# Optimization experiments

Hardware: AMD Instinct MI355X
Metric: run time of the kernel (lower is better)

## Reference

```python
import jax, jax.numpy as jnp
import numpy as np

# Module hyperparameters (n_heads must be 1 for the torch module's views to be consistent)
N_HEADS = 1
INPUT_DIM = 512
EMBED_DIM = 512
KEY_DIM = 512   # defaults: val_dim = embed_dim // n_heads, key_dim = val_dim
VAL_DIM = 512
INTERNAL = 80   # internal_node_holder
LEAF = 50       # leaf_node_holder
NEXT = 1        # next_holder
G = INTERNAL + LEAF + NEXT  # graph_size = 131
B = 512


def _uniform_init(k, shape):
    s = 1.0 / np.sqrt(shape[-1])
    return jax.random.uniform(k, shape, jnp.float32, -s, s)


def setup_inputs() -> dict:
    key = jax.random.key(0)
    ks = jax.random.split(key, 8)
    q = jax.random.normal(ks[0], (B * G, INPUT_DIM), jnp.float32)
    h = jax.random.normal(ks[1], (B, G, INPUT_DIM), jnp.float32)
    mask = jax.random.randint(ks[2], (B, G), 0, 2, jnp.int32)  # >0 means masked
    Wq = _uniform_init(ks[3], (KEY_DIM, INPUT_DIM))
    Wk = _uniform_init(ks[4], (KEY_DIM, INPUT_DIM))
    Wv = _uniform_init(ks[5], (VAL_DIM, INPUT_DIM))
    Wo = _uniform_init(ks[6], (EMBED_DIM, KEY_DIM))
    bo = _uniform_init(ks[7], (EMBED_DIM,))
    return {"q": q, "mask": mask, "graph_size": G, "evaluate": 0, "h": h,
            "Wq": Wq, "Wk": Wk, "Wv": Wv, "Wo": Wo, "bo": bo}


def reference(q, mask, graph_size, evaluate, h, Wq, Wk, Wv, Wo, bo):
    Gs = graph_size
    Bs = q.shape[0] // Gs
    norm = 1.0 / np.sqrt(KEY_DIM)

    # Projections (Linear, no bias). With n_heads=1 the (n_heads,B,N,-1) view is just (B,N,d).
    Q = (q @ Wq.T).reshape(Bs, Gs, KEY_DIM)                        # (B, G, dk)
    hflat = h.reshape(-1, INPUT_DIM)
    K = (hflat @ Wk.T).reshape(Bs, Gs, KEY_DIM)                    # (B, G, dk)
    V = (hflat @ Wv.T).reshape(Bs, Gs, VAL_DIM)                    # (B, G, dv)

    compatibility = norm * jnp.einsum('bqd,bkd->bqk', Q, K)       # (B, G, G)

    # mask (B,G) -> broadcast to (B,G,G); force the leaf-node block True
    idx = jnp.arange(Gs)
    mid = (idx >= INTERNAL) & (idx < Gs - NEXT)                    # leaf-node slots
    full_mask = (mask > 0)[:, None, :] | (mid[:, None] & mid[None, :])[None, :, :]

    fill = -jnp.inf if evaluate else -30.0
    compatibility = jnp.where(full_mask, fill, compatibility)
    attn = jax.nn.softmax(compatibility, axis=-1)
    attn = jnp.where(full_mask, 0.0, attn)                         # attnc zero-mask

    heads = jnp.einsum('bqk,bkd->bqd', attn, V)                    # (B, G, dv)
    out = heads.reshape(Bs * Gs, N_HEADS * VAL_DIM) @ Wo.T + bo    # (B*G, embed_dim)
    return out
```

## Files before the change

### kernel.cpp

```cpp
#include <hip/hip_runtime.h>
#include <hip/hip_bf16.h>

typedef short s16x8 __attribute__((ext_vector_type(8)));
typedef short s16x4 __attribute__((ext_vector_type(4)));
typedef float f32x4 __attribute__((ext_vector_type(4)));
typedef unsigned short u16;

#define MROWS 67072
#define GSZ   131
#define VT_KSTRIDE 160
#define VT_BATCH   (512 * VT_KSTRIDE)

__device__ inline u16 f2bf(float f) {
    return (u16)((__float_as_uint(f) + 0x8000u) >> 16);
}
__device__ inline unsigned pack2(float a, float b) {
    unsigned ua = __float_as_uint(a) + 0x8000u;
    unsigned ub = __float_as_uint(b) + 0x8000u;
    return (ua >> 16) | (ub & 0xFFFF0000u);
}
__device__ inline f32x4 mfma16(s16x8 a, s16x8 b, f32x4 c) {
    return __builtin_amdgcn_mfma_f32_16x16x32_bf16(a, b, c, 0, 0, 0);
}
typedef const __attribute__((address_space(1))) unsigned gas_u32;
typedef __attribute__((address_space(3))) unsigned las_u32;
__device__ inline void async16(const void* g, void* l) {
    __builtin_amdgcn_global_load_lds((gas_u32*)g, (las_u32*)l, 16, 0, 0);
}

__global__ __launch_bounds__(256)
void cvt_kernel(const float* __restrict__ src, u16* __restrict__ dst, int n8) {
    int i = blockIdx.x * 256 + threadIdx.x;
    if (i >= n8) return;
    const float4* s4 = (const float4*)src;
    float4 a = s4[2 * (size_t)i], b = s4[2 * (size_t)i + 1];
    union { s16x8 v; unsigned u[4]; } o;
    o.u[0] = pack2(a.x, a.y); o.u[1] = pack2(a.z, a.w);
    o.u[2] = pack2(b.x, b.y); o.u[3] = pack2(b.z, b.w);
    *(s16x8*)(dst + 8 * (size_t)i) = o.v;
}

template<int MODE>
__global__ __launch_bounds__(256, 2)
void gemm_bt(const u16* __restrict__ A, const u16* __restrict__ Bw,
             void* __restrict__ Outp, const float* __restrict__ bias)
{
    extern __shared__ __align__(16) char smem[];
    u16* smA = (u16*)smem;
    u16* smB = (u16*)(smem + 8192);
    u16* smC = (u16*)smem;

    const int tid  = threadIdx.x;
    const int lane = tid & 63;
    const int w    = tid >> 6;
    const int wm   = w >> 1, wn = w & 1;

    const int id    = (int)(blockIdx.x & 7) * 262 + (int)(blockIdx.x >> 3);
    const int mbase = (id >> 2) * 128;
    const int nbase = (id & 3) * 128;

    const int srow = w * 32 + (lane >> 2);
    const int scg  = (lane & 3) ^ (srow & 3);
    const u16* agp = A  + (size_t)(mbase + srow) * 512 + scg * 8;
    const u16* bgp = Bw + (size_t)(nbase + srow) * 512 + scg * 8;
    u16* al = smA + w * 1024;
    u16* bl = smB + w * 1024;

    f32x4 acc[4][4];
#pragma unroll
    for (int i = 0; i < 4; ++i)
#pragma unroll
        for (int j = 0; j < 4; ++j) acc[i][j] = (f32x4){0.f, 0.f, 0.f, 0.f};

    const int lr = lane & 15;
    const int co = ((lane >> 4) ^ (lr & 3)) * 8;

    for (int kk = 0; kk < 16; ++kk) {
        const int k0 = kk * 32;
        async16(agp + k0,            al);
        async16(agp + k0 + 16 * 512, al + 512);
        async16(bgp + k0,            bl);
        async16(bgp + k0 + 16 * 512, bl + 512);
        __syncthreads();

        s16x8 afr[4], bfr[4];
#pragma unroll
        for (int mi = 0; mi < 4; ++mi)
            afr[mi] = *(const s16x8*)&smA[(wm * 64 + mi * 16 + lr) * 32 + co];
#pragma unroll
        for (int ni = 0; ni < 4; ++ni)
            bfr[ni] = *(const s16x8*)&smB[(wn * 64 + ni * 16 + lr) * 32 + co];
#pragma unroll
        for (int mi = 0; mi < 4; ++mi)
#pragma unroll
            for (int ni = 0; ni < 4; ++ni)
                acc[mi][ni] = mfma16(afr[mi], bfr[ni], acc[mi][ni]);
        __syncthreads();
    }

    if constexpr (MODE == 2) {
        float bv[4];
#pragma unroll
        for (int ni = 0; ni < 4; ++ni) bv[ni] = bias[nbase + wn * 64 + ni * 16 + lr];
        float* outp = (float*)Outp;
#pragma unroll
        for (int mi = 0; mi < 4; ++mi)
#pragma unroll
            for (int ni = 0; ni < 4; ++ni) {
                int row0 = wm * 64 + mi * 16 + (lane >> 4) * 4;
                int col  = nbase + wn * 64 + ni * 16 + lr;
#pragma unroll
                for (int r = 0; r < 4; ++r)
                    outp[(size_t)(mbase + row0 + r) * 512 + col] = acc[mi][ni][r] + bv[ni];
            }
    } else if constexpr (MODE == 0) {
#pragma unroll
        for (int mi = 0; mi < 4; ++mi)
#pragma unroll
            for (int ni = 0; ni < 4; ++ni) {
                int row0 = wm * 64 + mi * 16 + (lane >> 4) * 4;
                int col  = wn * 64 + ni * 16 + lr;
#pragma unroll
                for (int r = 0; r < 4; ++r)
                    smC[(row0 + r) * 136 + col] = f2bf(acc[mi][ni][r]);
            }
        __syncthreads();
        u16* outp = (u16*)Outp;
        int rr = tid >> 1, cs = (tid & 1) * 64;
#pragma unroll
        for (int j = 0; j < 8; ++j) {
            s16x8 v = *(const s16x8*)&smC[rr * 136 + cs + j * 8];
            *(s16x8*)(outp + (size_t)(mbase + rr) * 512 + nbase + cs + j * 8) = v;
        }
    } else {
#pragma unroll
        for (int mi = 0; mi < 4; ++mi)
#pragma unroll
            for (int ni = 0; ni < 4; ++ni) {
                int nl = wn * 64 + ni * 16 + lr;
                int m0 = wm * 64 + mi * 16 + (lane >> 4) * 4;
                s16x4 pk;
#pragma unroll
                for (int r = 0; r < 4; ++r) pk[r] = (short)f2bf(acc[mi][ni][r]);
                *(s16x4*)&smC[nl * 136 + m0] = pk;
            }
        __syncthreads();
        u16* outp = (u16*)Outp;
        for (int i = 0; i < 32; ++i) {
            int n = w * 32 + i;
            int d = nbase + n;
#pragma unroll
            for (int hh = 0; hh < 2; ++hh) {
                int ml = hh * 64 + lane;
                unsigned mg = (unsigned)(mbase + ml);
                unsigned bb = mg / 131u;
                unsigned k2 = mg - bb * 131u;
                outp[(size_t)bb * VT_BATCH + (size_t)d * VT_KSTRIDE + k2] = smC[n * 136 + ml];
            }
        }
    }
}

__global__ __launch_bounds__(256, 4)
void attn_kernel(u16* __restrict__ QHb, const u16* __restrict__ Kb,
                 const u16* __restrict__ Vtb, const int* __restrict__ mask,
                 const int* __restrict__ evp)
{
    __shared__ __align__(16) u16 Qs[32 * 520];
    float* Ss = (float*)Qs;
    u16*   Ps = Qs + 9472;

    const int tid  = threadIdx.x;
    const int lane = tid & 63;
    const int w    = tid >> 6;
    const int id   = (int)(blockIdx.x & 7) * 320 + (int)(blockIdx.x >> 3);
    const int b    = id / 5;
    const int qt   = id - b * 5;
    const int q0   = qt * 32;
    const size_t rowbase = (size_t)b * GSZ;

    {
        int r = tid >> 3, cs = (tid & 7) * 64;
        int q = q0 + r;
        if (q < GSZ) {
            const u16* src = QHb + (rowbase + q) * 512 + cs;
#pragma unroll
            for (int j = 0; j < 8; ++j)
                *(s16x8*)&Qs[r * 520 + cs + j * 8] = *(const s16x8*)(src + j * 8);
        } else {
            s16x8 z = (s16x8){0,0,0,0,0,0,0,0};
#pragma unroll
            for (int j = 0; j < 8; ++j) *(s16x8*)&Qs[r * 520 + cs + j * 8] = z;
        }
    }
    __syncthreads();

    const int lr = lane & 15;
    const int lk = (lane >> 4) * 8;
    const float norm = 0.044194173824159216f;

    f32x4 sacc[3][2];
#pragma unroll
    for (int t = 0; t < 3; ++t) {
        sacc[t][0] = (f32x4){0.f,0.f,0.f,0.f};
        sacc[t][1] = (f32x4){0.f,0.f,0.f,0.f};
    }
#pragma unroll
    for (int t = 0; t < 3; ++t) {
        const int nt = w + 4 * t;
        if (nt < 9) {
            const u16* kbase = Kb + (rowbase + nt * 16 + lr) * 512 + lk;
#pragma unroll
            for (int ks = 0; ks < 16; ++ks) {
                s16x8 bfr = *(const s16x8*)(kbase + ks * 32);
                s16x8 a0  = *(const s16x8*)&Qs[(lr) * 520 + ks * 32 + lk];
                s16x8 a1  = *(const s16x8*)&Qs[(16 + lr) * 520 + ks * 32 + lk];
                sacc[t][0] = mfma16(a0, bfr, sacc[t][0]);
                sacc[t][1] = mfma16(a1, bfr, sacc[t][1]);
            }
        }
    }
    __syncthreads();

#pragma unroll
    for (int t = 0; t < 3; ++t) {
        const int nt = w + 4 * t;
        if (nt < 9) {
            int col = nt * 16 + lr;
            int rb  = (lane >> 4) * 4;
#pragma unroll
            for (int r = 0; r < 4; ++r) {
                Ss[(rb + r) * 148 + col]      = sacc[t][0][r] * norm;
                Ss[(16 + rb + r) * 148 + col] = sacc[t][1][r] * norm;
            }
        }
    }
    __syncthreads();

    {
        int r = tid >> 3, sub = tid & 7;
        int q = q0 + r;
        bool midq = (q >= 80) && (q < 130);
        int ev = *evp;
        float fill = ev ? -__builtin_inff() : -30.0f;
        float sv[17];
        float mx = -__builtin_inff();
#pragma unroll
        for (int j = 0; j < 17; ++j) {
            int k = sub + 8 * j;
            float s = -__builtin_inff();
            if (k < GSZ) {
                bool mk = (mask[b * GSZ + k] > 0) || (midq && (k >= 80) && (k < 130));
                s = mk ? fill : Ss[r * 148 + k];
            }
            sv[j] = s;
            mx = fmaxf(mx, s);
        }
#pragma unroll
        for (int off = 1; off < 8; off <<= 1) mx = fmaxf(mx, __shfl_xor(mx, off, 64));
        float sum = 0.f;
#pragma unroll
        for (int j = 0; j < 17; ++j) {
            int k = sub + 8 * j;
            if (k < GSZ) sum += __expf(sv[j] - mx);
        }
#pragma unroll
        for (int off = 1; off < 8; off <<= 1) sum += __shfl_xor(sum, off, 64);
        float inv = 1.0f / sum;
#pragma unroll
        for (int j = 0; j < 17; ++j) {
            int k = sub + 8 * j;
            if (k < GSZ) {
                bool mk = (mask[b * GSZ + k] > 0) || (midq && (k >= 80) && (k < 130));
                float p = mk ? 0.0f : __expf(sv[j] - mx) * inv;
                Ps[r * 168 + k] = f2bf(p);
            }
        }
        for (int k = GSZ + sub; k < 160; k += 8) Ps[r * 168 + k] = 0;
    }
    __syncthreads();

    f32x4 hacc[2][8];
#pragma unroll
    for (int mi = 0; mi < 2; ++mi)
#pragma unroll
        for (int ni = 0; ni < 8; ++ni) hacc[mi][ni] = (f32x4){0.f,0.f,0.f,0.f};
    const u16* vtbase = Vtb + (size_t)b * VT_BATCH + (size_t)(w * 128 + lr) * VT_KSTRIDE + lk;
#pragma unroll
    for (int kc = 0; kc < 5; ++kc) {
        s16x8 a0 = *(const s16x8*)&Ps[(lr) * 168 + kc * 32 + lk];
        s16x8 a1 = *(const s16x8*)&Ps[(16 + lr) * 168 + kc * 32 + lk];
#pragma unroll
        for (int ni = 0; ni < 8; ++ni) {
            s16x8 bfr = *(const s16x8*)(vtbase + (size_t)ni * 16 * VT_KSTRIDE + kc * 32);
            hacc[0][ni] = mfma16(a0, bfr, hacc[0][ni]);
            hacc[1][ni] = mfma16(a1, bfr, hacc[1][ni]);
        }
    }
    __syncthreads();

#pragma unroll
    for (int mi = 0; mi < 2; ++mi)
#pragma unroll
        for (int ni = 0; ni < 8; ++ni) {
            int row0 = mi * 16 + (lane >> 4) * 4;
            int col  = w * 128 + ni * 16 + lr;
#pragma unroll
            for (int r = 0; r < 4; ++r)
                Qs[(row0 + r) * 520 + col] = f2bf(hacc[mi][ni][r]);
        }
    __syncthreads();
    {
        int r = tid >> 3, cs = (tid & 7) * 64;
        int q = q0 + r;
        if (q < GSZ) {
            u16* dst = QHb + (rowbase + q) * 512 + cs;
#pragma unroll
            for (int j = 0; j < 8; ++j)
                *(s16x8*)(dst + j * 8) = *(const s16x8*)&Qs[r * 520 + cs + j * 8];
        }
    }
}

extern "C" void kernel_launch(void* const* d_in, const int* in_sizes, int n_in,
                              void* d_out, int out_size, void* d_ws, size_t ws_size,
                              hipStream_t stream) {
    const float* q    = (const float*)d_in[0];
    const int*   mask = (const int*)d_in[1];
    const int*   evp  = (const int*)d_in[3];
    const float* h    = (const float*)d_in[4];
    const float* Wq   = (const float*)d_in[5];
    const float* Wk   = (const float*)d_in[6];
    const float* Wv   = (const float*)d_in[7];
    const float* Wo   = (const float*)d_in[8];
    const float* bo   = (const float*)d_in[9];
    float* out = (float*)d_out;

    u16* Cbuf = (u16*)d_ws;
    u16* Kbuf = Cbuf + (size_t)MROWS * 512;
    u16* Qbuf = Kbuf + (size_t)MROWS * 512;
    u16* wWq  = Qbuf + (size_t)MROWS * 512;
    u16* wWk  = wWq + 512 * 512;
    u16* wWv  = wWk + 512 * 512;
    u16* wWo  = wWv + 512 * 512;
    u16* Vtb  = (u16*)d_out;

    const int n8_big = MROWS * 512 / 8;
    const int n8_w   = 512 * 512 / 8;
    dim3 bb(256);
    dim3 gcvt((n8_big + 255) / 256), gcw((n8_w + 255) / 256);
    dim3 gg(2096);
    const size_t lds_big = 34816, lds_min = 16384;

    cvt_kernel<<<gcw, bb, 0, stream>>>(Wq, wWq, n8_w);
    cvt_kernel<<<gcw, bb, 0, stream>>>(Wk, wWk, n8_w);
    cvt_kernel<<<gcw, bb, 0, stream>>>(Wv, wWv, n8_w);
    cvt_kernel<<<gcw, bb, 0, stream>>>(Wo, wWo, n8_w);

    cvt_kernel<<<gcvt, bb, 0, stream>>>(h, Cbuf, n8_big);
    gemm_bt<0><<<gg, bb, lds_big, stream>>>(Cbuf, wWk, (void*)Kbuf, nullptr);
    gemm_bt<1><<<gg, bb, lds_big, stream>>>(Cbuf, wWv, (void*)Vtb, nullptr);

    cvt_kernel<<<gcvt, bb, 0, stream>>>(q, Cbuf, n8_big);
    gemm_bt<0><<<gg, bb, lds_big, stream>>>(Cbuf, wWq, (void*)Qbuf, nullptr);

    attn_kernel<<<dim3(2560), bb, 0, stream>>>(Qbuf, Kbuf, Vtb, mask, evp);

    gemm_bt<2><<<gg, bb, lds_min, stream>>>(Qbuf, wWo, (void*)out, bo);
}
```

Baseline: 739.9 us.

## Prefetch K/V fragments and mask into registers in attention kernel

Loads the mask values into registers at kernel start, batches the K-fragment global loads eight at a time ahead of their MFMAs, and issues the first V-fragment loads before the softmax phase. The V loop is double-buffered so the next chunk is loaded while the current one is multiplied. Launch bounds drop from 4 to 3 blocks per SIMD to leave room for the extra registers, which may reduce occupancy.

```diff
diff --git a/kernel.cpp b/kernel.cpp
--- a/kernel.cpp
+++ b/kernel.cpp
@@ -161,7 +161,7 @@
     }
 }
 
-__global__ __launch_bounds__(256, 4)
+__global__ __launch_bounds__(256, 3)
 void attn_kernel(u16* __restrict__ QHb, const u16* __restrict__ Kb,
                  const u16* __restrict__ Vtb, const int* __restrict__ mask,
                  const int* __restrict__ evp)
@@ -179,18 +179,29 @@
     const int q0   = qt * 32;
     const size_t rowbase = (size_t)b * GSZ;
 
+    const int r8  = tid >> 3;
+    const int sub = tid & 7;
+
+    int ev = *evp;
+    int mkpre[17];
+#pragma unroll
+    for (int j = 0; j < 17; ++j) {
+        int k = sub + 8 * j;
+        mkpre[j] = (k < GSZ) ? mask[b * GSZ + k] : 1;
+    }
+
     {
-        int r = tid >> 3, cs = (tid & 7) * 64;
-        int q = q0 + r;
+        int cs = (tid & 7) * 64;
+        int q = q0 + r8;
         if (q < GSZ) {
             const u16* src = QHb + (rowbase + q) * 512 + cs;
 #pragma unroll
             for (int j = 0; j < 8; ++j)
-                *(s16x8*)&Qs[r * 520 + cs + j * 8] = *(const s16x8*)(src + j * 8);
+                *(s16x8*)&Qs[r8 * 520 + cs + j * 8] = *(const s16x8*)(src + j * 8);
         } else {
             s16x8 z = (s16x8){0,0,0,0,0,0,0,0};
 #pragma unroll
-            for (int j = 0; j < 8; ++j) *(s16x8*)&Qs[r * 520 + cs + j * 8] = z;
+            for (int j = 0; j < 8; ++j) *(s16x8*)&Qs[r8 * 520 + cs + j * 8] = z;
         }
     }
     __syncthreads();
@@ -198,6 +209,7 @@
     const int lr = lane & 15;
     const int lk = (lane >> 4) * 8;
     const float norm = 0.044194173824159216f;
+    const u16* vtbase = Vtb + (size_t)b * VT_BATCH + (size_t)(w * 128 + lr) * VT_KSTRIDE + lk;
 
     f32x4 sacc[3][2];
 #pragma unroll
@@ -211,15 +223,28 @@
         if (nt < 9) {
             const u16* kbase = Kb + (rowbase + nt * 16 + lr) * 512 + lk;
 #pragma unroll
-            for (int ks = 0; ks < 16; ++ks) {
-                s16x8 bfr = *(const s16x8*)(kbase + ks * 32);
-                s16x8 a0  = *(const s16x8*)&Qs[(lr) * 520 + ks * 32 + lk];
-                s16x8 a1  = *(const s16x8*)&Qs[(16 + lr) * 520 + ks * 32 + lk];
-                sacc[t][0] = mfma16(a0, bfr, sacc[t][0]);
-                sacc[t][1] = mfma16(a1, bfr, sacc[t][1]);
-            }
-        }
-    }
+            for (int h = 0; h < 2; ++h) {
+                s16x8 kf[8];
+#pragma unroll
+                for (int j = 0; j < 8; ++j)
+                    kf[j] = *(const s16x8*)(kbase + (h * 8 + j) * 32);
+#pragma unroll
+                for (int j = 0; j < 8; ++j) {
+                    const int ks = h * 8 + j;
+                    s16x8 a0 = *(const s16x8*)&Qs[(lr) * 520 + ks * 32 + lk];
+                    s16x8 a1 = *(const s16x8*)&Qs[(16 + lr) * 520 + ks * 32 + lk];
+                    sacc[t][0] = mfma16(a0, kf[j], sacc[t][0]);
+                    sacc[t][1] = mfma16(a1, kf[j], sacc[t][1]);
+                }
+            }
+        }
+    }
+
+    s16x8 vf[8];
+#pragma unroll
+    for (int j = 0; j < 8; ++j)
+        vf[j] = *(const s16x8*)(vtbase + (size_t)j * 16 * VT_KSTRIDE);
+
     __syncthreads();
 
 #pragma unroll
@@ -238,10 +263,8 @@
     __syncthreads();
 
     {
-        int r = tid >> 3, sub = tid & 7;
-        int q = q0 + r;
+        int q = q0 + r8;
         bool midq = (q >= 80) && (q < 130);
-        int ev = *evp;
         float fill = ev ? -__builtin_inff() : -30.0f;
         float sv[17];
         float mx = -__builtin_inff();
@@ -250,8 +273,8 @@
             int k = sub + 8 * j;
             float s = -__builtin_inff();
             if (k < GSZ) {
-                bool mk = (mask[b * GSZ + k] > 0) || (midq && (k >= 80) && (k < 130));
-                s = mk ? fill : Ss[r * 148 + k];
+                bool mk = (mkpre[j] > 0) || (midq && (k >= 80) && (k < 130));
+                s = mk ? fill : Ss[r8 * 148 + k];
             }
             sv[j] = s;
             mx = fmaxf(mx, s);
@@ -271,12 +294,12 @@
         for (int j = 0; j < 17; ++j) {
             int k = sub + 8 * j;
             if (k < GSZ) {
-                bool mk = (mask[b * GSZ + k] > 0) || (midq && (k >= 80) && (k < 130));
+                bool mk = (mkpre[j] > 0) || (midq && (k >= 80) && (k < 130));
                 float p = mk ? 0.0f : __expf(sv[j] - mx) * inv;
-                Ps[r * 168 + k] = f2bf(p);
-            }
-        }
-        for (int k = GSZ + sub; k < 160; k += 8) Ps[r * 168 + k] = 0;
+                Ps[r8 * 168 + k] = f2bf(p);
+            }
+        }
+        for (int k = GSZ + sub; k < 160; k += 8) Ps[r8 * 168 + k] = 0;
     }
     __syncthreads();
 
@@ -285,16 +308,24 @@
     for (int mi = 0; mi < 2; ++mi)
 #pragma unroll
         for (int ni = 0; ni < 8; ++ni) hacc[mi][ni] = (f32x4){0.f,0.f,0.f,0.f};
-    const u16* vtbase = Vtb + (size_t)b * VT_BATCH + (size_t)(w * 128 + lr) * VT_KSTRIDE + lk;
 #pragma unroll
     for (int kc = 0; kc < 5; ++kc) {
+        s16x8 vn[8];
+        if (kc < 4) {
+#pragma unroll
+            for (int j = 0; j < 8; ++j)
+                vn[j] = *(const s16x8*)(vtbase + (size_t)j * 16 * VT_KSTRIDE + (kc + 1) * 32);
+        }
         s16x8 a0 = *(const s16x8*)&Ps[(lr) * 168 + kc * 32 + lk];
         s16x8 a1 = *(const s16x8*)&Ps[(16 + lr) * 168 + kc * 32 + lk];
 #pragma unroll
         for (int ni = 0; ni < 8; ++ni) {
-            s16x8 bfr = *(const s16x8*)(vtbase + (size_t)ni * 16 * VT_KSTRIDE + kc * 32);
-            hacc[0][ni] = mfma16(a0, bfr, hacc[0][ni]);
-            hacc[1][ni] = mfma16(a1, bfr, hacc[1][ni]);
+            hacc[0][ni] = mfma16(a0, vf[ni], hacc[0][ni]);
+            hacc[1][ni] = mfma16(a1, vf[ni], hacc[1][ni]);
+        }
+        if (kc < 4) {
+#pragma unroll
+            for (int j = 0; j < 8; ++j) vf[j] = vn[j];
         }
     }
     __syncthreads();
@@ -311,13 +342,13 @@
         }
     __syncthreads();
     {
-        int r = tid >> 3, cs = (tid & 7) * 64;
-        int q = q0 + r;
+        int cs = (tid & 7) * 64;
+        int q = q0 + r8;
         if (q < GSZ) {
             u16* dst = QHb + (rowbase + q) * 512 + cs;
 #pragma unroll
             for (int j = 0; j < 8; ++j)
-                *(s16x8*)(dst + j * 8) = *(const s16x8*)&Qs[r * 520 + cs + j * 8];
+                *(s16x8*)(dst + j * 8) = *(const s16x8*)&Qs[r8 * 520 + cs + j * 8];
         }
     }
 }
```

Result: no change. 731.6 us (-1.1%).
